# Performance work log

Measured on AMD Instinct MI355X. Metric: run time of the kernel, lower is better.

Reference implementation:

```python
import jax, jax.numpy as jnp
import numpy as np
import math

D = 768
H = 8
DK = D // H
FF = 1024
EPS = 1e-5


def _layer_norm(x, g, b):
    m = jnp.mean(x, axis=-1, keepdims=True)
    v = jnp.mean((x - m) ** 2, axis=-1, keepdims=True)
    return (x - m) * jax.lax.rsqrt(v + EPS) * g + b


def _mha(x, attention_mask, Wq, bq, Wv, bv, g, b):
    # x: (B,S,D); attention_mask: (B,S,1) bool (True = masked/padding query row)
    B, S, _ = x.shape
    q = (x @ Wq + bq).reshape(B, S, H, DK).transpose(0, 2, 1, 3)  # (B,H,S,dk)
    # NOTE: original code uses the V projection for BOTH k and v (k = self.V(x))
    kv = (x @ Wv + bv).reshape(B, S, H, DK).transpose(0, 2, 1, 3)
    k = kv
    v = kv
    w = jnp.einsum('bhqd,bhkd->bhqk', q, k) / math.sqrt(DK)  # (B,H,S,S)
    pad = attention_mask[:, None, :, :]                      # (B,1,S,1) -> bcast (B,1,S,S)
    causal = jnp.triu(jnp.ones((S, S), dtype=bool), k=1)     # look-ahead mask
    mask = pad | causal
    w = jnp.where(mask, jnp.float32(-1e9), w)
    # NOTE: original uses nn.Softmax(dim=2) -> softmax over the QUERY axis
    score = jax.nn.softmax(w, axis=2)
    o = jnp.einsum('bhqk,bhkd->bhqd', score, v)              # (B,H,S,dk)
    o = o.transpose(0, 2, 1, 3).reshape(B, S, D)
    return _layer_norm(o + x, g, b)


def _ffn(x, W1, b1, W2, b2, g, b):
    h = jax.nn.relu(x @ W1 + b1)
    return _layer_norm(h @ W2 + b2 + x, g, b)


def setup_inputs() -> dict:
    key = jax.random.key(0)
    ks = jax.random.split(key, 16)
    B, S = 8, 1024
    sc = 0.02
    inp = {
        'x': jax.random.normal(ks[0], (B, S, D), dtype=jnp.float32),
        'attention_mask': jax.random.randint(ks[1], (B, S, 1), 0, 2).astype(bool),
    }
    for i, pre in enumerate(['a1', 'a2']):
        inp[pre + '_Wq'] = jax.random.normal(ks[2 + 4 * i], (D, D), dtype=jnp.float32) * sc
        inp[pre + '_bq'] = jnp.zeros((D,), dtype=jnp.float32)
        inp[pre + '_Wv'] = jax.random.normal(ks[3 + 4 * i], (D, D), dtype=jnp.float32) * sc
        inp[pre + '_bv'] = jnp.zeros((D,), dtype=jnp.float32)
        inp[pre + '_g'] = jnp.ones((D,), dtype=jnp.float32)
        inp[pre + '_b'] = jnp.zeros((D,), dtype=jnp.float32)
    inp['f_W1'] = jax.random.normal(ks[10], (D, FF), dtype=jnp.float32) * sc
    inp['f_b1'] = jnp.zeros((FF,), dtype=jnp.float32)
    inp['f_W2'] = jax.random.normal(ks[11], (FF, D), dtype=jnp.float32) * sc
    inp['f_b2'] = jnp.zeros((D,), dtype=jnp.float32)
    inp['f_g'] = jnp.ones((D,), dtype=jnp.float32)
    inp['f_b'] = jnp.zeros((D,), dtype=jnp.float32)
    return inp


def reference(x, attention_mask,
              a1_Wq, a1_bq, a1_Wv, a1_bv, a1_g, a1_b,
              a2_Wq, a2_bq, a2_Wv, a2_bv, a2_g, a2_b,
              f_W1, f_b1, f_W2, f_b2, f_g, f_b):
    x = _mha(x, attention_mask, a1_Wq, a1_bq, a1_Wv, a1_bv, a1_g, a1_b)
    x = _mha(x, attention_mask, a2_Wq, a2_bq, a2_Wv, a2_bv, a2_g, a2_b)
    x = _ffn(x, f_W1, f_b1, f_W2, f_b2, f_g, f_b)
    return x
```

## Files before the change

kernel.cpp:

```cpp
#include <hip/hip_runtime.h>
#include <cstddef>

#define BB 8
#define SS 1024
#define DD 768
#define HH 8
#define DKK 96
#define FFF 1024
#define MM (BB*SS)
#define QVW 1536
#define SM_SCALE 0.10206207261596577f
#define NT2 8

typedef unsigned short ushort_t;
typedef short short8 __attribute__((ext_vector_type(8)));
typedef float f32x4 __attribute__((ext_vector_type(4)));
typedef float f32x16 __attribute__((ext_vector_type(16)));
typedef ushort_t us4 __attribute__((ext_vector_type(4)));
typedef unsigned uint2v __attribute__((ext_vector_type(2)));

__device__ __forceinline__ ushort_t f2b(float f) {
    union { float f; unsigned u; } x; x.f = f;
    unsigned r = x.u + 0x7fffu + ((x.u >> 16) & 1u);
    return (ushort_t)(r >> 16);
}
__device__ __forceinline__ float b2f(ushort_t u) {
    union { unsigned u; float f; } x; x.u = ((unsigned)u) << 16;
    return x.f;
}
__device__ __forceinline__ void gload16(const ushort_t* g, void* lds_base) {
    __builtin_amdgcn_global_load_lds(
        (const __attribute__((address_space(1))) unsigned int*)g,
        (__attribute__((address_space(3))) unsigned int*)lds_base, 16, 0, 0);
}
__device__ __forceinline__ void plswap(unsigned& a, unsigned& b) {
#if __has_builtin(__builtin_amdgcn_permlane32_swap)
    uint2v r = __builtin_amdgcn_permlane32_swap(a, b, false, false);
    a = r[0]; b = r[1];
#else
    asm("v_permlane32_swap_b32 %0, %1" : "+v"(a), "+v"(b));
#endif
}

__device__ __forceinline__ void castWT_body(
    const float* __restrict__ W, ushort_t* __restrict__ Wt,
    int K, int N, int bx, int by)
{
    __shared__ float T[32][33];
    const int tx = threadIdx.x & 31, ty = threadIdx.x >> 5;
    const int n0 = bx * 32, k0 = by * 32;
    #pragma unroll
    for (int r = 0; r < 4; ++r)
        T[ty + 8*r][tx] = W[(size_t)(k0 + ty + 8*r) * N + n0 + tx];
    __syncthreads();
    #pragma unroll
    for (int r = 0; r < 4; ++r)
        Wt[(size_t)(n0 + ty + 8*r) * K + k0 + tx] = f2b(T[tx][ty + 8*r]);
}

__global__ __launch_bounds__(256) void prep_all(
    const float* __restrict__ Wqa, const float* __restrict__ Wva,
    const float* __restrict__ Wqb, const float* __restrict__ Wvb,
    ushort_t* __restrict__ Tqa, ushort_t* __restrict__ Tva,
    ushort_t* __restrict__ Tqb, ushort_t* __restrict__ Tvb,
    const float* __restrict__ W1, ushort_t* __restrict__ T1,
    const float* __restrict__ W2, ushort_t* __restrict__ T2,
    const float* __restrict__ x, ushort_t* __restrict__ xb)
{
    const int id = blockIdx.x;
    if (id < 2304) {
        const int z = id / 576, r = id % 576;
        const float* W = (z == 0) ? Wqa : (z == 1) ? Wva : (z == 2) ? Wqb : Wvb;
        ushort_t* Wt   = (z == 0) ? Tqa : (z == 1) ? Tva : (z == 2) ? Tqb : Tvb;
        castWT_body(W, Wt, DD, DD, r % 24, r / 24);
    } else if (id < 3072) {
        const int r = id - 2304;
        castWT_body(W1, T1, DD, FFF, r % 32, r / 32);
    } else if (id < 3840) {
        const int r = id - 3072;
        castWT_body(W2, T2, FFF, DD, r % 24, r / 24);
    } else {
        const int i = (id - 3840) * 256 + threadIdx.x;
        const float4 v = ((const float4*)x)[i];
        us4 o; o.x = f2b(v.x); o.y = f2b(v.y); o.z = f2b(v.z); o.w = f2b(v.w);
        ((us4*)xb)[i] = o;
    }
}

template<int RELU, int WVT>
__global__ __launch_bounds__(256) void gemm_bt(
    const ushort_t* __restrict__ A, const ushort_t* __restrict__ Bt,
    const float* __restrict__ bias, const float* __restrict__ bias2, int bN,
    ushort_t* __restrict__ C, int K, int N, ushort_t* __restrict__ Vt)
{
    __shared__ ushort_t S[128*136];
    ushort_t* As = S;
    ushort_t* Bs = S + 128*64;
    const int tid  = threadIdx.x;
    const int lane = tid & 63, wave = tid >> 6;
    const int wm = wave >> 1, wn = wave & 1;
    const int n = lane & 15, quad = lane >> 4;
    const int sx = n & 7;
    const int nbx = N >> 7;
    const int cpx = gridDim.x >> 3;
    const int sw  = (blockIdx.x & 7) * cpx + (blockIdx.x >> 3);
    const int bm = (sw / nbx) * 128, bn = (sw % nbx) * 128;

    f32x4 acc[4][4];
    #pragma unroll
    for (int i = 0; i < 4; ++i)
        #pragma unroll
        for (int j = 0; j < 4; ++j) acc[i][j] = (f32x4){0.f, 0.f, 0.f, 0.f};

    for (int k0 = 0; k0 < K; k0 += 64) {
        #pragma unroll
        for (int it = 0; it < 4; ++it) {
            const int u   = (it*4 + wave)*64 + lane;
            const int row = u >> 3;
            const int c   = (u & 7) ^ (row & 7);
            gload16(A  + (size_t)(bm + row) * K + k0 + c*8, (char*)As + (it*4 + wave)*1024);
            gload16(Bt + (size_t)(bn + row) * K + k0 + c*8, (char*)Bs + (it*4 + wave)*1024);
        }
        __syncthreads();
        #pragma unroll
        for (int ks = 0; ks < 2; ++ks) {
            short8 af[4], bf[4];
            #pragma unroll
            for (int i = 0; i < 4; ++i)
                af[i] = *(short8*)&As[((wm*64 + i*16 + n)*8 + ((ks*4 + quad) ^ sx))*8];
            #pragma unroll
            for (int j = 0; j < 4; ++j)
                bf[j] = *(short8*)&Bs[((wn*64 + j*16 + n)*8 + ((ks*4 + quad) ^ sx))*8];
            __builtin_amdgcn_s_setprio(1);
            #pragma unroll
            for (int i = 0; i < 4; ++i)
                #pragma unroll
                for (int j = 0; j < 4; ++j)
                    acc[i][j] = __builtin_amdgcn_mfma_f32_16x16x32_bf16(af[i], bf[j], acc[i][j], 0, 0, 0);
            __builtin_amdgcn_s_setprio(0);
        }
        __syncthreads();
    }
    #pragma unroll
    for (int j = 0; j < 4; ++j) {
        const int col = wn*64 + j*16 + n;
        const int gcol = bn + col;
        const float bsv = (gcol < bN) ? bias[gcol] : bias2[gcol - bN];
        #pragma unroll
        for (int i = 0; i < 4; ++i) {
            const int lrow = wm*64 + i*16 + quad*4;
            #pragma unroll
            for (int r = 0; r < 4; ++r) {
                float v = acc[i][j][r] + bsv;
                if (RELU) v = fmaxf(v, 0.f);
                S[(lrow + r)*136 + col] = f2b(v);
            }
        }
        if (WVT && bn >= DD) {
            const int gkv = gcol - DD;
            const int hh = gkv / DKK, dk = gkv % DKK;
            ushort_t* vt = Vt + ((size_t)((bm >> 10)*HH + hh)*DKK + dk)*SS + (bm & 1023);
            #pragma unroll
            for (int i = 0; i < 4; ++i) {
                us4 o;
                o.x = f2b(acc[i][j][0] + bsv);
                o.y = f2b(acc[i][j][1] + bsv);
                o.z = f2b(acc[i][j][2] + bsv);
                o.w = f2b(acc[i][j][3] + bsv);
                *(us4*)(vt + wm*64 + i*16 + quad*4) = o;
            }
        }
    }
    __syncthreads();
    #pragma unroll
    for (int it = 0; it < 8; ++it) {
        const int u = it*256 + tid;
        const int grow = u >> 4, gc = u & 15;
        *(short8*)(C + (size_t)(bm + grow)*N + bn + gc*8) = *(short8*)&S[grow*136 + gc*8];
    }
}

__global__ __launch_bounds__(512) void attn_sums(
    const ushort_t* __restrict__ QV, const int* __restrict__ amask,
    float* __restrict__ lpart)
{
    __shared__ ushort_t Qs[128*128];
    __shared__ ushort_t Ks[2][64*128];
    __shared__ float colsum[2][8][64];
    const int tid = threadIdx.x, lane = tid & 63, wave = tid >> 6;
    const int n = lane & 15, quad = lane >> 4, sx = n & 7;
    const int hwid = blockIdx.x;
    const int v = (hwid & 7) * 32 + (hwid >> 3);
    const int px = v & 3, h = (v >> 2) & 7, b = v >> 5;
    const ushort_t* Qh = QV + (size_t)b*SS*QVW + h*DKK;
    const ushort_t* Kh = QV + (size_t)b*SS*QVW + DD + h*DKK;
    float* lpq = lpart + (size_t)(b*HH + h)*NT2*SS;

    #pragma unroll
    for (int half = 0; half < 2; ++half) {
        const int qt2 = half ? (7 - px) : px;
        const int q0 = qt2 * 128;
        const int ktmax = 2*qt2 + 1;
        #pragma unroll
        for (int it = 0; it < 4; ++it) {
            const int u = (it*8 + wave)*64 + lane;
            const int row = u >> 4, c = (u & 15) ^ (row & 7);
            if (c < 12)
                gload16(Qh + (size_t)(q0 + row)*QVW + c*8, (char*)Qs + (it*8 + wave)*1024);
        }
        const int4 mv = *(const int4*)&amask[b*SS + q0 + wave*16 + quad*4];
        const int mr[4] = {mv.x, mv.y, mv.z, mv.w};
        #pragma unroll
        for (int it = 0; it < 2; ++it) {
            const int u = (it*8 + wave)*64 + lane;
            const int row = u >> 4, c = (u & 15) ^ (row & 7);
            if (c < 12)
                gload16(Kh + (size_t)row*QVW + c*8, (char*)Ks[0] + (it*8 + wave)*1024);
        }
        __syncthreads();
        short8 aq[3];
        #pragma unroll
        for (int ks = 0; ks < 3; ++ks)
            aq[ks] = *(short8*)&Qs[((wave*16 + n)*16 + ((ks*4 + quad) ^ sx))*8];

        int cur = 0;
        for (int kt = 0; kt <= ktmax; ++kt) {
            const int k0 = kt * 64;
            if (kt < ktmax) {
                #pragma unroll
                for (int it = 0; it < 2; ++it) {
                    const int u = (it*8 + wave)*64 + lane;
                    const int row = u >> 4, c = (u & 15) ^ (row & 7);
                    if (c < 12)
                        gload16(Kh + (size_t)(k0 + 64 + row)*QVW + c*8,
                                (char*)Ks[cur^1] + (it*8 + wave)*1024);
                }
            }
            if (kt > 0 && tid < 64) {
                const float s = colsum[cur^1][0][tid] + colsum[cur^1][1][tid]
                              + colsum[cur^1][2][tid] + colsum[cur^1][3][tid]
                              + colsum[cur^1][4][tid] + colsum[cur^1][5][tid]
                              + colsum[cur^1][6][tid] + colsum[cur^1][7][tid];
                lpq[(size_t)qt2*SS + (k0 - 64) + tid] = s;
            }
            #pragma unroll
            for (int ns = 0; ns < 4; ++ns) {
                f32x4 sa = (f32x4){0.f, 0.f, 0.f, 0.f};
                __builtin_amdgcn_s_setprio(1);
                #pragma unroll
                for (int ks = 0; ks < 3; ++ks) {
                    const short8 bk = *(short8*)&Ks[cur][((ns*16 + n)*16 + ((ks*4 + quad) ^ sx))*8];
                    sa = __builtin_amdgcn_mfma_f32_16x16x32_bf16(aq[ks], bk, sa, 0, 0, 0);
                }
                __builtin_amdgcn_s_setprio(0);
                const int kl = ns*16 + n;
                const int keyg = k0 + kl;
                float s = 0.f;
                #pragma unroll
                for (int r = 0; r < 4; ++r) {
                    const int qg = q0 + wave*16 + quad*4 + r;
                    const bool dead = (mr[r] != 0) || (keyg > qg);
                    s += dead ? 0.f : __expf(sa[r] * SM_SCALE);
                }
                s += __shfl_xor(s, 16);
                s += __shfl_xor(s, 32);
                if (quad == 0) colsum[cur][wave][kl] = s;
            }
            __syncthreads();
            cur ^= 1;
        }
        if (tid < 64) {
            const int pb = ktmax & 1;
            const float s = colsum[pb][0][tid] + colsum[pb][1][tid]
                          + colsum[pb][2][tid] + colsum[pb][3][tid]
                          + colsum[pb][4][tid] + colsum[pb][5][tid]
                          + colsum[pb][6][tid] + colsum[pb][7][tid];
            lpq[(size_t)qt2*SS + ktmax*64 + tid] = s;
        }
    }
}

__global__ __launch_bounds__(256) void mk_rl(
    const float* __restrict__ lpart, float* __restrict__ rl)
{
    const int bh = blockIdx.x;
    const float* lp = lpart + (size_t)bh*NT2*SS;
    const int k = threadIdx.x * 4;
    const int qtmin = k >> 7;
    float4 l = {0.f, 0.f, 0.f, 0.f};
    for (int q = qtmin; q < NT2; ++q) {
        const float4 v = *(const float4*)(lp + (size_t)q*SS + k);
        l.x += v.x; l.y += v.y; l.z += v.z; l.w += v.w;
    }
    float4 r;
    r.x = (l.x > 0.f) ? (1.f / l.x) : 0.f;
    r.y = (l.y > 0.f) ? (1.f / l.y) : 0.f;
    r.z = (l.z > 0.f) ? (1.f / l.z) : 0.f;
    r.w = (l.w > 0.f) ? (1.f / l.w) : 0.f;
    *(float4*)(rl + (size_t)bh*SS + k) = r;
}

__global__ __launch_bounds__(256, 3) void attn_pv_re(
    const ushort_t* __restrict__ QV, const int* __restrict__ amask,
    const ushort_t* __restrict__ Vt, const float* __restrict__ rl,
    ushort_t* __restrict__ O)
{
    __shared__ ushort_t Ks[2][64*128];
    __shared__ ushort_t Vs[96*64];
    const int tid = threadIdx.x, lane = tid & 63, wave = tid >> 6;
    const int ln31 = lane & 31, hi = lane >> 5;
    const int hwid = blockIdx.x;
    const int v = (hwid & 7) * 32 + (hwid >> 3);
    const int px = v & 3, h = (v >> 2) & 7, b = v >> 5;
    const ushort_t* Qh = QV + (size_t)b*SS*QVW + h*DKK;
    const ushort_t* Kh = QV + (size_t)b*SS*QVW + DD + h*DKK;
    const ushort_t* Vth = Vt + ((size_t)b*HH + h)*DKK*SS;
    const float* rlh = rl + ((size_t)b*HH + h)*SS;

    #pragma unroll
    for (int half = 0; half < 2; ++half) {
        const int qt2 = half ? (7 - px) : px;
        const int q0 = qt2 * 128;
        const int ktmax = 2*qt2 + 1;
        const int qrow = q0 + wave*32 + ln31;
        short8 bq[6];
        #pragma unroll
        for (int t = 0; t < 6; ++t)
            bq[t] = *(const short8*)(Qh + (size_t)qrow*QVW + t*16 + hi*8);
        const bool padq = amask[b*SS + qrow] != 0;

        #pragma unroll
        for (int it = 0; it < 4; ++it) {
            const int u = (it*4 + wave)*64 + lane;
            const int row = u >> 4, c = (u & 15) ^ (row & 7);
            if (c < 12)
                gload16(Kh + (size_t)row*QVW + c*8, (char*)Ks[0] + (it*4 + wave)*1024);
        }
        #pragma unroll
        for (int it = 0; it < 3; ++it) {
            const int u = (it*4 + wave)*64 + lane;
            const int row = u >> 3, c = (u & 7) ^ (row & 7);
            gload16(Vth + (size_t)row*SS + c*8, (char*)Vs + (it*4 + wave)*1024);
        }
        __syncthreads();

        f32x16 acc[3];
        #pragma unroll
        for (int db = 0; db < 3; ++db)
            #pragma unroll
            for (int i = 0; i < 16; ++i) acc[db][i] = 0.f;

        int cur = 0;
        for (int kt = 0; kt <= ktmax; ++kt) {
            const int k0 = kt * 64;
            if (kt < ktmax) {
                #pragma unroll
                for (int it = 0; it < 4; ++it) {
                    const int u = (it*4 + wave)*64 + lane;
                    const int row = u >> 4, c = (u & 15) ^ (row & 7);
                    if (c < 12)
                        gload16(Kh + (size_t)(k0 + 64 + row)*QVW + c*8,
                                (char*)Ks[cur^1] + (it*4 + wave)*1024);
                }
            }
            unsigned wv[2][8];
            #pragma unroll
            for (int kb = 0; kb < 2; ++kb) {
                f32x16 sk;
                #pragma unroll
                for (int i = 0; i < 16; ++i) sk[i] = 0.f;
                const int krow = kb*32 + ln31;
                __builtin_amdgcn_s_setprio(1);
                #pragma unroll
                for (int t = 0; t < 6; ++t) {
                    const short8 ak = *(short8*)&Ks[cur][krow*128 + (((t*2 + hi) ^ (krow & 7))*8)];
                    sk = __builtin_amdgcn_mfma_f32_32x32x16_bf16(ak, bq[t], sk, 0, 0, 0);
                }
                __builtin_amdgcn_s_setprio(0);
                const int kbase = k0 + kb*32 + 4*hi;
                float4 r4[4];
                #pragma unroll
                for (int m = 0; m < 4; ++m)
                    r4[m] = *(const float4*)(rlh + kbase + 8*m);
                float p[16];
                #pragma unroll
                for (int r = 0; r < 16; ++r) {
                    const int kg = kbase + (r & 3) + 8*(r >> 2);
                    const bool dead = padq || (kg > qrow);
                    const float rs = (&r4[r >> 2].x)[r & 3];
                    p[r] = dead ? 0.f : __expf(sk[r] * SM_SCALE) * rs;
                }
                #pragma unroll
                for (int i = 0; i < 8; ++i)
                    asm("v_cvt_pk_bf16_f32 %0, %1, %2" : "=v"(wv[kb][i]) : "v"(p[2*i]), "v"(p[2*i+1]));
                plswap(wv[kb][0], wv[kb][2]);
                plswap(wv[kb][1], wv[kb][3]);
                plswap(wv[kb][4], wv[kb][6]);
                plswap(wv[kb][5], wv[kb][7]);
            }
            __syncthreads();
            __builtin_amdgcn_s_setprio(1);
            #pragma unroll
            for (int kb = 0; kb < 2; ++kb) {
                #pragma unroll
                for (int s = 0; s < 2; ++s) {
                    short8 ae;
                    unsigned* aeu = (unsigned*)&ae;
                    aeu[0] = wv[kb][s*4 + 0]; aeu[1] = wv[kb][s*4 + 1];
                    aeu[2] = wv[kb][s*4 + 2]; aeu[3] = wv[kb][s*4 + 3];
                    #pragma unroll
                    for (int db = 0; db < 3; ++db) {
                        const int drow = db*32 + ln31;
                        const short8 bv = *(short8*)&Vs[drow*64 + (((kb*4 + s*2 + hi) ^ (drow & 7))*8)];
                        acc[db] = __builtin_amdgcn_mfma_f32_32x32x16_bf16(ae, bv, acc[db], 0, 0, 0);
                    }
                }
            }
            __builtin_amdgcn_s_setprio(0);
            __syncthreads();
            if (kt < ktmax) {
                #pragma unroll
                for (int it = 0; it < 3; ++it) {
                    const int u = (it*4 + wave)*64 + lane;
                    const int row = u >> 3, c = (u & 7) ^ (row & 7);
                    gload16(Vth + (size_t)row*SS + k0 + 64 + c*8, (char*)Vs + (it*4 + wave)*1024);
                }
            }
            cur ^= 1;
        }
        #pragma unroll
        for (int db = 0; db < 3; ++db) {
            #pragma unroll
            for (int r = 0; r < 16; ++r) {
                const int q = q0 + wave*32 + (r & 3) + 8*(r >> 2) + 4*hi;
                O[((size_t)b*SS + q)*DD + h*DKK + db*32 + ln31] = f2b(acc[db][r]);
            }
        }
    }
}

__device__ __forceinline__ float block_sum256(float s, float* tmp4)
{
    #pragma unroll
    for (int off = 32; off > 0; off >>= 1) s += __shfl_down(s, off);
    __syncthreads();
    if ((threadIdx.x & 63) == 0) tmp4[threadIdx.x >> 6] = s;
    __syncthreads();
    return tmp4[0] + tmp4[1] + tmp4[2] + tmp4[3];
}

template<int XBF, int RBF, int OUTF32>
__global__ __launch_bounds__(256) void resid_ln(
    const void* __restrict__ X, const void* __restrict__ R,
    const float* __restrict__ g, const float* __restrict__ beta,
    ushort_t* __restrict__ OutB, float* __restrict__ OutF)
{
    __shared__ float tmp4[4];
    const int row = blockIdx.x;
    const int tid = threadIdx.x;
    float v[3], s = 0.f;
    #pragma unroll
    for (int i = 0; i < 3; ++i) {
        const size_t idx = (size_t)row * DD + tid + 256*i;
        const float xv = XBF ? b2f(((const ushort_t*)X)[idx]) : ((const float*)X)[idx];
        const float rv = RBF ? b2f(((const ushort_t*)R)[idx]) : ((const float*)R)[idx];
        v[i] = xv + rv;
        s += v[i];
    }
    const float mu = block_sum256(s, tmp4) * (1.f / DD);
    float qv = 0.f;
    #pragma unroll
    for (int i = 0; i < 3; ++i) { const float d = v[i] - mu; qv += d * d; }
    const float inv = rsqrtf(block_sum256(qv, tmp4) * (1.f / DD) + 1e-5f);
    #pragma unroll
    for (int i = 0; i < 3; ++i) {
        const int c = tid + 256*i;
        const float o = (v[i] - mu) * inv * g[c] + beta[c];
        if (OUTF32) OutF[(size_t)row * DD + c] = o;
        else        OutB[(size_t)row * DD + c] = f2b(o);
    }
}

extern "C" void kernel_launch(void* const* d_in, const int* in_sizes, int n_in,
                              void* d_out, int out_size, void* d_ws, size_t ws_size,
                              hipStream_t stream)
{
    (void)in_sizes; (void)n_in; (void)out_size; (void)ws_size;
    const float* x0    = (const float*)d_in[0];
    const int*   amask = (const int*)d_in[1];
    const float* a1_Wq = (const float*)d_in[2];
    const float* a1_bq = (const float*)d_in[3];
    const float* a1_Wv = (const float*)d_in[4];
    const float* a1_bv = (const float*)d_in[5];
    const float* a1_g  = (const float*)d_in[6];
    const float* a1_b  = (const float*)d_in[7];
    const float* a2_Wq = (const float*)d_in[8];
    const float* a2_bq = (const float*)d_in[9];
    const float* a2_Wv = (const float*)d_in[10];
    const float* a2_bv = (const float*)d_in[11];
    const float* a2_g  = (const float*)d_in[12];
    const float* a2_b  = (const float*)d_in[13];
    const float* f_W1  = (const float*)d_in[14];
    const float* f_b1  = (const float*)d_in[15];
    const float* f_W2  = (const float*)d_in[16];
    const float* f_b2  = (const float*)d_in[17];
    const float* f_g   = (const float*)d_in[18];
    const float* f_b   = (const float*)d_in[19];

    char* ws = (char*)d_ws;
    size_t off = 0;
    auto alloc = [&](size_t bytes) { void* p = ws + off; off += (bytes + 255) & ~(size_t)255; return p; };
    ushort_t* WqvT1 = (ushort_t*)alloc((size_t)QVW*DD*2);
    ushort_t* WqvT2 = (ushort_t*)alloc((size_t)QVW*DD*2);
    ushort_t* W1T   = (ushort_t*)alloc((size_t)DD*FFF*2);
    ushort_t* W2T   = (ushort_t*)alloc((size_t)DD*FFF*2);
    ushort_t* xb0   = (ushort_t*)alloc((size_t)MM*DD*2);
    ushort_t* xb1   = (ushort_t*)alloc((size_t)MM*DD*2);
    ushort_t* xb2   = (ushort_t*)alloc((size_t)MM*DD*2);
    ushort_t* Ob    = (ushort_t*)alloc((size_t)MM*DD*2);
    ushort_t* QVb   = (ushort_t*)alloc((size_t)MM*QVW*2);
    ushort_t* hb    = QVb;
    ushort_t* Vtb   = (ushort_t*)alloc((size_t)MM*DD*2);
    float* lpart = (float*)alloc((size_t)BB*HH*NT2*SS*4);
    float* rlb   = (float*)alloc((size_t)BB*HH*SS*4);
    float* out = (float*)d_out;

    const dim3 blk(256);
    const dim3 blk512(512);
    const dim3 gat(256);

    prep_all<<<dim3(9984), blk, 0, stream>>>(
        a1_Wq, a1_Wv, a2_Wq, a2_Wv,
        WqvT1, WqvT1 + (size_t)DD*DD, WqvT2, WqvT2 + (size_t)DD*DD,
        f_W1, W1T, f_W2, W2T, x0, xb0);

    gemm_bt<0,1><<<dim3((QVW/128)*(MM/128)), blk, 0, stream>>>(xb0, WqvT1, a1_bq, a1_bv, DD, QVb, DD, QVW, Vtb);
    attn_sums<<<gat, blk512, 0, stream>>>(QVb, amask, lpart);
    mk_rl<<<dim3(BB*HH), blk, 0, stream>>>(lpart, rlb);
    attn_pv_re<<<gat, blk, 0, stream>>>(QVb, amask, Vtb, rlb, Ob);
    resid_ln<1,0,0><<<dim3(MM), blk, 0, stream>>>(Ob, x0, a1_g, a1_b, xb1, nullptr);

    gemm_bt<0,1><<<dim3((QVW/128)*(MM/128)), blk, 0, stream>>>(xb1, WqvT2, a2_bq, a2_bv, DD, QVb, DD, QVW, Vtb);
    attn_sums<<<gat, blk512, 0, stream>>>(QVb, amask, lpart);
    mk_rl<<<dim3(BB*HH), blk, 0, stream>>>(lpart, rlb);
    attn_pv_re<<<gat, blk, 0, stream>>>(QVb, amask, Vtb, rlb, Ob);
    resid_ln<1,1,0><<<dim3(MM), blk, 0, stream>>>(Ob, xb1, a2_g, a2_b, xb2, nullptr);

    gemm_bt<1,0><<<dim3((FFF/128)*(MM/128)), blk, 0, stream>>>(xb2, W1T, f_b1, f_b1, FFF, hb, DD, FFF, nullptr);
    gemm_bt<0,0><<<dim3((DD/128)*(MM/128)), blk, 0, stream>>>(hb, W2T, f_b2, f_b2, DD, Ob, FFF, DD, nullptr);
    resid_ln<1,1,1><<<dim3(MM), blk, 0, stream>>>(Ob, xb2, f_g, f_b, nullptr, out);
}
```

Measured before the change: 446.2 us.

## Double-buffer V tiles in attention PV kernel and interleave QK/PV per subblock

Makes the V shared-memory tile double-buffered so the next V tile is prefetched together with the next K tile at the top of each iteration, instead of after a second barrier. It also merges the QK-score and PV MFMA phases per 32-key sub-block, removing one __syncthreads per iteration and the wv staging array. In exchange, shared memory rises (extra 12 KB) and launch bounds drop from 3 to 2 blocks per CU, which may lower occupancy.

```diff
diff --git a/kernel.cpp b/kernel.cpp
--- a/kernel.cpp
+++ b/kernel.cpp
@@ -300,13 +300,13 @@
     *(float4*)(rl + (size_t)bh*SS + k) = r;
 }
 
-__global__ __launch_bounds__(256, 3) void attn_pv_re(
+__global__ __launch_bounds__(256, 2) void attn_pv_re(
     const ushort_t* __restrict__ QV, const int* __restrict__ amask,
     const ushort_t* __restrict__ Vt, const float* __restrict__ rl,
     ushort_t* __restrict__ O)
 {
     __shared__ ushort_t Ks[2][64*128];
-    __shared__ ushort_t Vs[96*64];
+    __shared__ ushort_t Vs[2][96*64];
     const int tid = threadIdx.x, lane = tid & 63, wave = tid >> 6;
     const int ln31 = lane & 31, hi = lane >> 5;
     const int hwid = blockIdx.x;
@@ -340,7 +340,7 @@
         for (int it = 0; it < 3; ++it) {
             const int u = (it*4 + wave)*64 + lane;
             const int row = u >> 3, c = (u & 7) ^ (row & 7);
-            gload16(Vth + (size_t)row*SS + c*8, (char*)Vs + (it*4 + wave)*1024);
+            gload16(Vth + (size_t)row*SS + c*8, (char*)Vs[0] + (it*4 + wave)*1024);
         }
         __syncthreads();
 
@@ -362,8 +362,14 @@
                         gload16(Kh + (size_t)(k0 + 64 + row)*QVW + c*8,
                                 (char*)Ks[cur^1] + (it*4 + wave)*1024);
                 }
-            }
-            unsigned wv[2][8];
+                #pragma unroll
+                for (int it = 0; it < 3; ++it) {
+                    const int u = (it*4 + wave)*64 + lane;
+                    const int row = u >> 3, c = (u & 7) ^ (row & 7);
+                    gload16(Vth + (size_t)row*SS + k0 + 64 + c*8,
+                            (char*)Vs[cur^1] + (it*4 + wave)*1024);
+                }
+            }
             #pragma unroll
             for (int kb = 0; kb < 2; ++kb) {
                 f32x16 sk;
@@ -390,42 +396,31 @@
                     const float rs = (&r4[r >> 2].x)[r & 3];
                     p[r] = dead ? 0.f : __expf(sk[r] * SM_SCALE) * rs;
                 }
+                unsigned w[8];
                 #pragma unroll
                 for (int i = 0; i < 8; ++i)
-                    asm("v_cvt_pk_bf16_f32 %0, %1, %2" : "=v"(wv[kb][i]) : "v"(p[2*i]), "v"(p[2*i+1]));
-                plswap(wv[kb][0], wv[kb][2]);
-                plswap(wv[kb][1], wv[kb][3]);
-                plswap(wv[kb][4], wv[kb][6]);
-                plswap(wv[kb][5], wv[kb][7]);
-            }
-            __syncthreads();
-            __builtin_amdgcn_s_setprio(1);
-            #pragma unroll
-            for (int kb = 0; kb < 2; ++kb) {
+                    asm("v_cvt_pk_bf16_f32 %0, %1, %2" : "=v"(w[i]) : "v"(p[2*i]), "v"(p[2*i+1]));
+                plswap(w[0], w[2]);
+                plswap(w[1], w[3]);
+                plswap(w[4], w[6]);
+                plswap(w[5], w[7]);
+                __builtin_amdgcn_s_setprio(1);
                 #pragma unroll
                 for (int s = 0; s < 2; ++s) {
                     short8 ae;
                     unsigned* aeu = (unsigned*)&ae;
-                    aeu[0] = wv[kb][s*4 + 0]; aeu[1] = wv[kb][s*4 + 1];
-                    aeu[2] = wv[kb][s*4 + 2]; aeu[3] = wv[kb][s*4 + 3];
+                    aeu[0] = w[s*4 + 0]; aeu[1] = w[s*4 + 1];
+                    aeu[2] = w[s*4 + 2]; aeu[3] = w[s*4 + 3];
                     #pragma unroll
                     for (int db = 0; db < 3; ++db) {
                         const int drow = db*32 + ln31;
-                        const short8 bv = *(short8*)&Vs[drow*64 + (((kb*4 + s*2 + hi) ^ (drow & 7))*8)];
+                        const short8 bv = *(short8*)&Vs[cur][drow*64 + (((kb*4 + s*2 + hi) ^ (drow & 7))*8)];
                         acc[db] = __builtin_amdgcn_mfma_f32_32x32x16_bf16(ae, bv, acc[db], 0, 0, 0);
                     }
                 }
-            }
-            __builtin_amdgcn_s_setprio(0);
+                __builtin_amdgcn_s_setprio(0);
+            }
             __syncthreads();
-            if (kt < ktmax) {
-                #pragma unroll
-                for (int it = 0; it < 3; ++it) {
-                    const int u = (it*4 + wave)*64 + lane;
-                    const int row = u >> 3, c = (u & 7) ^ (row & 7);
-                    gload16(Vth + (size_t)row*SS + k0 + 64 + c*8, (char*)Vs + (it*4 + wave)*1024);
-                }
-            }
             cur ^= 1;
         }
         #pragma unroll
```

Measured after the change: 414.2 us. -7.2%, faster.
